# Kernel optimization log

Hardware: AMD Instinct MI355X
Metric: run time of the kernel (lower is better)

The kernel has to match this reference:

```python
import jax, jax.numpy as jnp
import numpy as np

B = 1024        # graphs per batch
NPG = 64        # nodes per graph (uniform)
DEG = 16        # avg degree
NE_PG = 256     # candidate non-edges per graph
N = B * NPG
E = N * DEG
NE = B * NE_PG
EMB, HID, NCAT, NET, NOUT = 64, 128, 100, 4, 101  # NOUT = num_external + 1


def setup_inputs() -> dict:
    key = jax.random.key(0)
    ks = jax.random.split(key, 32)
    rn = lambda k, shape: jax.random.normal(k, shape, jnp.float32) * 0.05
    # graph structure: edges and non-edges stay within each graph's node block
    x = jax.random.randint(ks[0], (N,), 0, NCAT)
    offs = jnp.repeat(jnp.arange(B) * NPG, NPG * DEG)
    src = jax.random.randint(ks[1], (E,), 0, NPG) + offs
    dst = jax.random.randint(ks[2], (E,), 0, NPG) + offs
    edge_index = jnp.stack([src, dst])
    edge_attr = jax.random.randint(ks[3], (E,), 0, NET)
    offs_ne = jnp.repeat(jnp.arange(B) * NPG, NE_PG)
    non_edges = jax.random.randint(ks[4], (NE, 2), 0, NPG) + offs_ne[:, None]
    batch = jnp.repeat(jnp.arange(B), NPG)
    return dict(
        node_tab=rn(ks[5], (NCAT, EMB)), edge_tab=rn(ks[6], (NET, EMB)),
        c1_w=rn(ks[7], (EMB, HID)), c1_we=rn(ks[8], (EMB, HID)),
        c1_as=rn(ks[9], (HID,)), c1_ad=rn(ks[10], (HID,)), c1_ae=rn(ks[11], (HID,)), c1_b=rn(ks[12], (HID,)),
        c2_w=rn(ks[13], (HID, HID)), c2_we=rn(ks[14], (EMB, HID)),
        c2_as=rn(ks[15], (HID,)), c2_ad=rn(ks[16], (HID,)), c2_ae=rn(ks[17], (HID,)), c2_b=rn(ks[18], (HID,)),
        s_w1=rn(ks[19], (HID, HID)), s_b1=rn(ks[20], (HID,)), s_w2=rn(ks[21], (HID, 1)), s_b2=rn(ks[22], (1,)),
        n_w1=rn(ks[23], (HID, HID)), n_b1=rn(ks[24], (HID,)), n_w2=rn(ks[25], (HID, NOUT)), n_b2=rn(ks[26], (NOUT,)),
        e_w1=rn(ks[27], (HID, HID)), e_b1=rn(ks[28], (HID,)), e_w2=rn(ks[29], (HID, 1)), e_b2=rn(ks[30], (1,)),
        x=x, edge_index=edge_index, edge_attr=edge_attr, non_edges=non_edges, batch=batch,
    )


def _gat(h_in, src, dst, e, W, We, a_s, a_d, a_e, b):
    """PyG GATConv, heads=1: gather -> leakyrelu logits -> segment softmax over dst -> scatter sum."""
    n = h_in.shape[0]
    h = h_in @ W                  # [N, C]
    he = e @ We                   # [E, C]
    logit = (h @ a_s)[src] + (h @ a_d)[dst] + he @ a_e   # [E]
    logit = jnp.where(logit > 0, logit, 0.2 * logit)      # leaky_relu(0.2)
    m = jax.ops.segment_max(logit, dst, num_segments=n)
    ex = jnp.exp(logit - m[dst])
    den = jax.ops.segment_sum(ex, dst, num_segments=n)
    alpha = ex / (den[dst] + 1e-16)
    return jax.ops.segment_sum(h[src] * alpha[:, None], dst, num_segments=n) + b


def _mlp(z, w1, b1, w2, b2):
    return jax.nn.relu(z @ w1 + b1) @ w2 + b2


def reference(node_tab, edge_tab,
              c1_w, c1_we, c1_as, c1_ad, c1_ae, c1_b,
              c2_w, c2_we, c2_as, c2_ad, c2_ae, c2_b,
              s_w1, s_b1, s_w2, s_b2,
              n_w1, n_b1, n_w2, n_b2,
              e_w1, e_b1, e_w2, e_b2,
              x, edge_index, edge_attr, non_edges, batch):
    src, dst = edge_index[0], edge_index[1]
    e = edge_tab[edge_attr]                      # [E, EMB]
    h = node_tab[x]                              # [N, EMB]
    h = jax.nn.relu(_gat(h, src, dst, e, c1_w, c1_we, c1_as, c1_ad, c1_ae, c1_b))
    h = _gat(h, src, dst, e, c2_w, c2_we, c2_as, c2_ad, c2_ae, c2_b)   # [N, HID]
    g = jax.ops.segment_sum(h, batch, num_segments=B)                   # [B, HID]
    stop = _mlp(g, s_w1, s_b1, s_w2, s_b2)                              # [B, 1]
    addnode = _mlp(h, n_w1, n_b1, n_w2, n_b2)                           # [N, NOUT]
    pair = h[non_edges[:, 0]] + h[non_edges[:, 1]]                      # [NE, HID]
    addedge = _mlp(pair, e_w1, e_b1, e_w2, e_b2)                        # [NE, 1]
    # uniform per-graph sizes -> the torch split/pad is a static reshape+concat
    return jnp.concatenate(
        [stop, addnode.reshape(B, NPG * NOUT), addedge.reshape(B, NE_PG)], axis=1)
```

## Files before the change

### kernel.cpp

```cpp
#include <hip/hip_runtime.h>


#define NPG 64
#define EPG 1024
#define NEPG 256
#define B_GR 1024
#define E_TOT 1048576
#define EMB 64
#define HID 128
#define NOUT 101
#define OUT_PG 6721

typedef __attribute__((ext_vector_type(8))) short bf16x8;
typedef __attribute__((ext_vector_type(4))) float f32x4;
typedef unsigned short ushort_t;

__device__ ushort_t g_c1w[EMB*HID];
__device__ ushort_t g_c2w[HID*HID];
__device__ ushort_t g_nw1[HID*HID];
__device__ ushort_t g_ew1[HID*HID];
__device__ ushort_t g_nw2[HID*112];
__device__ float    g_sw1t[HID*HID];
__device__ float    g_he1[4], g_he2[4];

__device__ __forceinline__ ushort_t f2bf(float f) {
  unsigned u = __float_as_uint(f);
  return (ushort_t)((u + 0x7fffu + ((u >> 16) & 1u)) >> 16);
}
__device__ __forceinline__ float bf2f(ushort_t h) {
  return __uint_as_float(((unsigned)h) << 16);
}

__global__ void prep_kernel(
    const float* __restrict__ edge_tab,
    const float* __restrict__ c1_w,  const float* __restrict__ c1_we,
    const float* __restrict__ c1_ae,
    const float* __restrict__ c2_w,  const float* __restrict__ c2_we,
    const float* __restrict__ c2_ae,
    const float* __restrict__ s_w1,  const float* __restrict__ n_w1,
    const float* __restrict__ n_w2,  const float* __restrict__ e_w1)
{
  const int b = blockIdx.x, tid = threadIdx.x;
  if (b == 0) {
    __shared__ float v1[EMB], v2[EMB];
    if (tid < EMB) {
      float a = 0.f, d = 0.f;
      for (int j = 0; j < HID; ++j) {
        a = fmaf(c1_we[tid*HID + j], c1_ae[j], a);
        d = fmaf(c2_we[tid*HID + j], c2_ae[j], d);
      }
      v1[tid] = a; v2[tid] = d;
    }
    __syncthreads();
    if (tid < 4) {
      float a = 0.f, d = 0.f;
      for (int k = 0; k < EMB; ++k) {
        const float ev = edge_tab[tid*EMB + k];
        a = fmaf(ev, v1[k], a); d = fmaf(ev, v2[k], d);
      }
      g_he1[tid] = a; g_he2[tid] = d;
    }
  } else if (b == 1) {
    for (int idx = tid; idx < EMB*HID; idx += 256) {
      const int j = idx & 7, l = (idx >> 3) & 63, r2 = idx >> 9;
      const int ks = r2 & 1, ct = r2 >> 1;
      const int row = ks*32 + (l >> 4)*8 + j;
      const int col = ct*16 + (l & 15);
      g_c1w[idx] = f2bf(c1_w[row*HID + col]);
    }
  } else if (b >= 2 && b <= 4) {
    const float* W = (b == 2) ? c2_w : (b == 3) ? n_w1 : e_w1;
    ushort_t* G = (b == 2) ? g_c2w : (b == 3) ? g_nw1 : g_ew1;
    for (int idx = tid; idx < HID*HID; idx += 256) {
      const int j = idx & 7, l = (idx >> 3) & 63, r2 = idx >> 9;
      const int ks = r2 & 3, ct = r2 >> 2;
      const int row = ks*32 + (l >> 4)*8 + j;
      const int col = ct*16 + (l & 15);
      G[idx] = f2bf(W[row*HID + col]);
    }
  } else if (b == 5) {
    for (int idx = tid; idx < HID*112; idx += 256) {
      const int j = idx & 7, l = (idx >> 3) & 63, r2 = idx >> 9;
      const int ks = r2 & 3, ct = r2 >> 2;
      const int row = ks*32 + (l >> 4)*8 + j;
      const int col = ct*16 + (l & 15);
      g_nw2[idx] = (col < NOUT) ? f2bf(n_w2[row*NOUT + col]) : (ushort_t)0;
    }
  } else {
    for (int idx = tid; idx < HID*HID; idx += 256)
      g_sw1t[idx] = s_w1[(idx & 127)*HID + (idx >> 7)];
  }
}

#define S_HC  0
#define S_R   18432
#define S_TP  35840
#define S_DEN 37888
#define S_NS  38144
#define S_ND  38400
#define S_XS  38656
#define S_GP  38912
#define S_ZH  39424
#define S_HCC 39936
#define S_TOT 39968

__global__ __launch_bounds__(256, 4) void graph_kernel(
    const float* __restrict__ node_tab,
    const float* __restrict__ c1_as, const float* __restrict__ c1_ad,
    const float* __restrict__ c1_b,
    const float* __restrict__ c2_as, const float* __restrict__ c2_ad,
    const float* __restrict__ c2_b,
    const float* __restrict__ s_b1,  const float* __restrict__ s_w2,
    const float* __restrict__ s_b2,
    const float* __restrict__ n_b1,  const float* __restrict__ n_b2,
    const float* __restrict__ e_b1,  const float* __restrict__ e_w2,
    const float* __restrict__ e_b2,
    const int* __restrict__ x,  const int* __restrict__ ei,
    const int* __restrict__ ea, const int* __restrict__ nedg,
    float* __restrict__ out)
{
  const int tid = threadIdx.x;
  const int gid = blockIdx.x;
  const int nb = gid * NPG;
  const int lane = tid & 63;
  const int wv = tid >> 6;
  const int qd = lane >> 4;
  const int cl = lane & 15;
  const int rb = wv * 16;

  __shared__ __align__(16) char smem[S_TOT];
  ushort_t* Hc   = (ushort_t*)(smem + S_HC);
  ushort_t* Ae   = (ushort_t*)(smem + S_R);
  float*    Pf   = (float*)   (smem + S_R);
  ushort_t* Pb   = (ushort_t*)(smem + S_R);
  ushort_t* Hr   = (ushort_t*)(smem + S_R);
  ushort_t* topo = (ushort_t*)(smem + S_TP);
  float*    part = (float*)   (smem + S_TP);
  float*    den  = (float*)   (smem + S_DEN);
  float*    ns   = (float*)   (smem + S_NS);
  float*    nd   = (float*)   (smem + S_ND);
  int*      xs   = (int*)     (smem + S_XS);
  float*    gp   = (float*)   (smem + S_GP);
  float*    zh   = (float*)   (smem + S_ZH);
  float*    hc   = (float*)   (smem + S_HCC);
  ushort_t* a1b  = Hc;

  for (int k = tid; k < EPG; k += 256) {
    const int s = ei[gid*EPG + k] - nb;
    const int d = ei[E_TOT + gid*EPG + k] - nb;
    const int t = ea[gid*EPG + k];
    topo[k] = (ushort_t)(s | (d << 6) | (t << 12));
  }
  if (tid < NPG) xs[tid] = x[nb + tid];
  if (tid >= 64 && tid < 72) hc[tid-64] = (tid < 68) ? g_he1[tid-64] : g_he2[tid-68];
  if (tid >= 128) gp[tid-128] = 0.f;
  __syncthreads();

  {
    const int n = tid >> 2;
    const int f0 = (tid & 3) * 16;
    const float* src = node_tab + xs[n]*EMB + f0;
    const float4 v0 = ((const float4*)src)[0];
    const float4 v1 = ((const float4*)src)[1];
    const float4 v2 = ((const float4*)src)[2];
    const float4 v3 = ((const float4*)src)[3];
    bf16x8 o0, o1;
    o0[0]=f2bf(v0.x); o0[1]=f2bf(v0.y); o0[2]=f2bf(v0.z); o0[3]=f2bf(v0.w);
    o0[4]=f2bf(v1.x); o0[5]=f2bf(v1.y); o0[6]=f2bf(v1.z); o0[7]=f2bf(v1.w);
    o1[0]=f2bf(v2.x); o1[1]=f2bf(v2.y); o1[2]=f2bf(v2.z); o1[3]=f2bf(v2.w);
    o1[4]=f2bf(v3.x); o1[5]=f2bf(v3.y); o1[6]=f2bf(v3.z); o1[7]=f2bf(v3.w);
    *(bf16x8*)(Ae + n*72 + f0)     = o0;
    *(bf16x8*)(Ae + n*72 + f0 + 8) = o1;
  }
  __syncthreads();

  {
    const bf16x8 af0 = *(const bf16x8*)(Ae + (rb+cl)*72 + qd*8);
    const bf16x8 af1 = *(const bf16x8*)(Ae + (rb+cl)*72 + 32 + qd*8);
    float pns[4] = {0.f,0.f,0.f,0.f}, pnd[4] = {0.f,0.f,0.f,0.f};
    #pragma unroll
    for (int ct = 0; ct < 8; ++ct) {
      f32x4 acc = {0.f, 0.f, 0.f, 0.f};
      const bf16x8 b0 = *(const bf16x8*)(g_c1w + ((ct*2+0)*64 + lane)*8);
      const bf16x8 b1 = *(const bf16x8*)(g_c1w + ((ct*2+1)*64 + lane)*8);
      acc = __builtin_amdgcn_mfma_f32_16x16x32_bf16(af0, b0, acc, 0, 0, 0);
      acc = __builtin_amdgcn_mfma_f32_16x16x32_bf16(af1, b1, acc, 0, 0, 0);
      const int n = ct*16 + cl;
      const float asv = c1_as[n], adv = c1_ad[n];
      #pragma unroll
      for (int r = 0; r < 4; ++r) {
        const float v = acc[r];
        Hc[n*72 + (rb + qd*4 + r)] = f2bf(v);
        pns[r] = fmaf(v, asv, pns[r]);
        pnd[r] = fmaf(v, adv, pnd[r]);
      }
    }
    #pragma unroll
    for (int r = 0; r < 4; ++r) {
      #pragma unroll
      for (int off = 1; off < 16; off <<= 1) {
        pns[r] += __shfl_xor(pns[r], off, 64);
        pnd[r] += __shfl_xor(pnd[r], off, 64);
      }
    }
    if (cl == 0) {
      #pragma unroll
      for (int r = 0; r < 4; ++r) { ns[rb+qd*4+r] = pns[r]; nd[rb+qd*4+r] = pnd[r]; }
    }
  }
  __syncthreads();

  {
    float4* pz = (float4*)Pf;
    #pragma unroll
    for (int j = 0; j < 4; ++j) pz[tid + j*256] = make_float4(0.f,0.f,0.f,0.f);
    if (tid < NPG) den[tid] = 0.f;
  }
  __syncthreads();

  for (int k = tid; k < EPG; k += 256) {
    const int tp = topo[k];
    const int s = tp & 63, d = (tp >> 6) & 63, t = tp >> 12;
    float l = ns[s] + nd[d] + hc[t];
    l = (l > 0.f) ? l : 0.2f * l;
    const float ex = __expf(l);
    atomicAdd(&den[d], ex);
    atomicAdd(&Pf[d*64 + s], ex);
  }
  __syncthreads();

  {
    float vreg[16];
    #pragma unroll
    for (int j = 0; j < 16; ++j) vreg[j] = Pf[tid + j*256];
    __syncthreads();
    #pragma unroll
    for (int j = 0; j < 16; ++j) {
      const int i = tid + j*256;
      Pb[(i >> 6)*72 + (i & 63)] = f2bf(vreg[j]);
    }
  }
  __syncthreads();

  {
    const bf16x8 a0 = *(const bf16x8*)(Pb + (rb+cl)*72 + qd*8);
    const bf16x8 a1 = *(const bf16x8*)(Pb + (rb+cl)*72 + 32 + qd*8);
    float inv4[4];
    #pragma unroll
    for (int r = 0; r < 4; ++r) inv4[r] = 1.f / (den[rb+qd*4+r] + 1e-16f);
    __syncthreads();
    #pragma unroll
    for (int ct = 0; ct < 8; ++ct) {
      f32x4 acc = {0.f, 0.f, 0.f, 0.f};
      const bf16x8 b0 = *(const bf16x8*)(Hc + (ct*16+cl)*72 + qd*8);
      const bf16x8 b1 = *(const bf16x8*)(Hc + (ct*16+cl)*72 + 32 + qd*8);
      acc = __builtin_amdgcn_mfma_f32_16x16x32_bf16(a0, b0, acc, 0, 0, 0);
      acc = __builtin_amdgcn_mfma_f32_16x16x32_bf16(a1, b1, acc, 0, 0, 0);
      const int n = ct*16 + cl;
      const float bias = c1_b[n];
      #pragma unroll
      for (int r = 0; r < 4; ++r)
        Hr[(rb + qd*4 + r)*136 + n] = f2bf(fmaxf(fmaf(acc[r], inv4[r], bias), 0.f));
    }
  }
  __syncthreads();

  {
    bf16x8 af[4];
    #pragma unroll
    for (int ks = 0; ks < 4; ++ks)
      af[ks] = *(const bf16x8*)(Hr + (rb+cl)*136 + ks*32 + qd*8);
    float pns[4] = {0.f,0.f,0.f,0.f}, pnd[4] = {0.f,0.f,0.f,0.f};
    #pragma unroll
    for (int ct = 0; ct < 8; ++ct) {
      f32x4 acc = {0.f, 0.f, 0.f, 0.f};
      #pragma unroll
      for (int ks = 0; ks < 4; ++ks) {
        const bf16x8 b = *(const bf16x8*)(g_c2w + ((ct*4+ks)*64 + lane)*8);
        acc = __builtin_amdgcn_mfma_f32_16x16x32_bf16(af[ks], b, acc, 0, 0, 0);
      }
      const int n = ct*16 + cl;
      const float asv = c2_as[n], adv = c2_ad[n];
      #pragma unroll
      for (int r = 0; r < 4; ++r) {
        const float v = acc[r];
        Hc[n*72 + (rb + qd*4 + r)] = f2bf(v);
        pns[r] = fmaf(v, asv, pns[r]);
        pnd[r] = fmaf(v, adv, pnd[r]);
      }
    }
    #pragma unroll
    for (int r = 0; r < 4; ++r) {
      #pragma unroll
      for (int off = 1; off < 16; off <<= 1) {
        pns[r] += __shfl_xor(pns[r], off, 64);
        pnd[r] += __shfl_xor(pnd[r], off, 64);
      }
    }
    if (cl == 0) {
      #pragma unroll
      for (int r = 0; r < 4; ++r) { ns[rb+qd*4+r] = pns[r]; nd[rb+qd*4+r] = pnd[r]; }
    }
  }
  __syncthreads();

  {
    float4* pz = (float4*)Pf;
    #pragma unroll
    for (int j = 0; j < 4; ++j) pz[tid + j*256] = make_float4(0.f,0.f,0.f,0.f);
    if (tid < NPG) den[tid] = 0.f;
  }
  __syncthreads();

  for (int k = tid; k < EPG; k += 256) {
    const int tp = topo[k];
    const int s = tp & 63, d = (tp >> 6) & 63, t = tp >> 12;
    float l = ns[s] + nd[d] + hc[4 + t];
    l = (l > 0.f) ? l : 0.2f * l;
    const float ex = __expf(l);
    atomicAdd(&den[d], ex);
    atomicAdd(&Pf[d*64 + s], ex);
  }
  __syncthreads();

  {
    float vreg[16];
    #pragma unroll
    for (int j = 0; j < 16; ++j) vreg[j] = Pf[tid + j*256];
    __syncthreads();
    #pragma unroll
    for (int j = 0; j < 16; ++j) {
      const int i = tid + j*256;
      Pb[(i >> 6)*72 + (i & 63)] = f2bf(vreg[j]);
    }
  }
  __syncthreads();

  {
    const bf16x8 a0 = *(const bf16x8*)(Pb + (rb+cl)*72 + qd*8);
    const bf16x8 a1 = *(const bf16x8*)(Pb + (rb+cl)*72 + 32 + qd*8);
    float inv4[4];
    #pragma unroll
    for (int r = 0; r < 4; ++r) inv4[r] = 1.f / (den[rb+qd*4+r] + 1e-16f);
    __syncthreads();
    #pragma unroll
    for (int ct = 0; ct < 8; ++ct) {
      f32x4 acc = {0.f, 0.f, 0.f, 0.f};
      const bf16x8 b0 = *(const bf16x8*)(Hc + (ct*16+cl)*72 + qd*8);
      const bf16x8 b1 = *(const bf16x8*)(Hc + (ct*16+cl)*72 + 32 + qd*8);
      acc = __builtin_amdgcn_mfma_f32_16x16x32_bf16(a0, b0, acc, 0, 0, 0);
      acc = __builtin_amdgcn_mfma_f32_16x16x32_bf16(a1, b1, acc, 0, 0, 0);
      const int n = ct*16 + cl;
      const float bias = c2_b[n];
      float colsum = 0.f;
      #pragma unroll
      for (int r = 0; r < 4; ++r) {
        const float v = fmaf(acc[r], inv4[r], bias);
        Hr[(rb + qd*4 + r)*136 + n] = f2bf(v);
        colsum += v;
      }
      colsum += __shfl_xor(colsum, 16, 64);
      colsum += __shfl_xor(colsum, 32, 64);
      if (qd == 0) atomicAdd(&gp[n], colsum);
    }
  }
  __syncthreads();

  {
    const int j = tid & 127, half = tid >> 7;
    const float* wr = g_sw1t + j*HID + half*64;
    const float* gr = gp + half*64;
    float p = 0.f;
    #pragma unroll
    for (int q = 0; q < 16; ++q) {
      const float4 w = ((const float4*)wr)[q];
      const float4 g = ((const float4*)gr)[q];
      p = fmaf(w.x, g.x, p); p = fmaf(w.y, g.y, p);
      p = fmaf(w.z, g.z, p); p = fmaf(w.w, g.w, p);
    }
    part[tid] = p;
  }
  __syncthreads();
  if (tid < HID) zh[tid] = fmaxf(part[tid] + part[tid+128] + s_b1[tid], 0.f);
  __syncthreads();
  if (tid < 64) {
    float p = fmaf(zh[tid], s_w2[tid], zh[tid+64]*s_w2[tid+64]);
    #pragma unroll
    for (int off = 32; off > 0; off >>= 1) p += __shfl_down(p, off, 64);
    if (tid == 0) out[(size_t)gid*OUT_PG] = p + s_b2[0];
  }
  __syncthreads();

  {
    bf16x8 af[4];
    #pragma unroll
    for (int ks = 0; ks < 4; ++ks)
      af[ks] = *(const bf16x8*)(Hr + (rb+cl)*136 + ks*32 + qd*8);
    #pragma unroll
    for (int ct = 0; ct < 8; ++ct) {
      f32x4 acc = {0.f, 0.f, 0.f, 0.f};
      #pragma unroll
      for (int ks = 0; ks < 4; ++ks) {
        const bf16x8 b = *(const bf16x8*)(g_nw1 + ((ct*4+ks)*64 + lane)*8);
        acc = __builtin_amdgcn_mfma_f32_16x16x32_bf16(af[ks], b, acc, 0, 0, 0);
      }
      const int n = ct*16 + cl;
      const float bias = n_b1[n];
      #pragma unroll
      for (int r = 0; r < 4; ++r)
        a1b[(rb + qd*4 + r)*136 + n] = f2bf(fmaxf(acc[r] + bias, 0.f));
    }
  }
  __syncthreads();

  {
    bf16x8 af[4];
    #pragma unroll
    for (int ks = 0; ks < 4; ++ks)
      af[ks] = *(const bf16x8*)(a1b + (rb+cl)*136 + ks*32 + qd*8);
    float* ob = out + (size_t)gid*OUT_PG + 1;
    #pragma unroll
    for (int ct = 0; ct < 7; ++ct) {
      f32x4 acc = {0.f, 0.f, 0.f, 0.f};
      #pragma unroll
      for (int ks = 0; ks < 4; ++ks) {
        const bf16x8 b = *(const bf16x8*)(g_nw2 + ((ct*4+ks)*64 + lane)*8);
        acc = __builtin_amdgcn_mfma_f32_16x16x32_bf16(af[ks], b, acc, 0, 0, 0);
      }
      const int o = ct*16 + cl;
      if (o < NOUT) {
        const float b2 = n_b2[o];
        #pragma unroll
        for (int r = 0; r < 4; ++r)
          ob[(size_t)(rb + qd*4 + r)*NOUT + o] = acc[r] + b2;
      }
    }
  }
  __syncthreads();

  if (tid < HID) { gp[tid] = e_b1[tid]; zh[tid] = e_w2[tid]; }
  {
    bf16x8 af[4];
    #pragma unroll
    for (int ks = 0; ks < 4; ++ks)
      af[ks] = *(const bf16x8*)(Hr + (rb+cl)*136 + ks*32 + qd*8);
    #pragma unroll
    for (int ct = 0; ct < 8; ++ct) {
      f32x4 acc = {0.f, 0.f, 0.f, 0.f};
      #pragma unroll
      for (int ks = 0; ks < 4; ++ks) {
        const bf16x8 b = *(const bf16x8*)(g_ew1 + ((ct*4+ks)*64 + lane)*8);
        acc = __builtin_amdgcn_mfma_f32_16x16x32_bf16(af[ks], b, acc, 0, 0, 0);
      }
      const int n = ct*16 + cl;
      #pragma unroll
      for (int r = 0; r < 4; ++r)
        a1b[(rb + qd*4 + r)*136 + n] = f2bf(acc[r]);
    }
  }
  __syncthreads();

  {
    const int2 pr = *(const int2*)(nedg + 2*(gid*NEPG + tid));
    const ushort_t* ui = a1b + (pr.x - nb)*136;
    const ushort_t* uj = a1b + (pr.y - nb)*136;
    float ssum = 0.f;
    #pragma unroll
    for (int q8 = 0; q8 < 16; ++q8) {
      const bf16x8 va = *(const bf16x8*)(ui + q8*8);
      const bf16x8 vb = *(const bf16x8*)(uj + q8*8);
      #pragma unroll
      for (int j = 0; j < 8; ++j) {
        const int c = q8*8 + j;
        float v = bf2f((ushort_t)va[j]) + bf2f((ushort_t)vb[j]) + gp[c];
        v = fmaxf(v, 0.f);
        ssum = fmaf(v, zh[c], ssum);
      }
    }
    out[(size_t)gid*OUT_PG + 1 + NPG*NOUT + tid] = ssum + e_b2[0];
  }
}

extern "C" void kernel_launch(void* const* d_in, const int* in_sizes, int n_in,
                              void* d_out, int out_size, void* d_ws, size_t ws_size,
                              hipStream_t stream) {
  const float* node_tab = (const float*)d_in[0];
  const float* edge_tab = (const float*)d_in[1];
  const float* c1_w  = (const float*)d_in[2];
  const float* c1_we = (const float*)d_in[3];
  const float* c1_as = (const float*)d_in[4];
  const float* c1_ad = (const float*)d_in[5];
  const float* c1_ae = (const float*)d_in[6];
  const float* c1_b  = (const float*)d_in[7];
  const float* c2_w  = (const float*)d_in[8];
  const float* c2_we = (const float*)d_in[9];
  const float* c2_as = (const float*)d_in[10];
  const float* c2_ad = (const float*)d_in[11];
  const float* c2_ae = (const float*)d_in[12];
  const float* c2_b  = (const float*)d_in[13];
  const float* s_w1  = (const float*)d_in[14];
  const float* s_b1  = (const float*)d_in[15];
  const float* s_w2  = (const float*)d_in[16];
  const float* s_b2  = (const float*)d_in[17];
  const float* n_w1  = (const float*)d_in[18];
  const float* n_b1  = (const float*)d_in[19];
  const float* n_w2  = (const float*)d_in[20];
  const float* n_b2  = (const float*)d_in[21];
  const float* e_w1  = (const float*)d_in[22];
  const float* e_b1  = (const float*)d_in[23];
  const float* e_w2  = (const float*)d_in[24];
  const float* e_b2  = (const float*)d_in[25];
  const int* x    = (const int*)d_in[26];
  const int* ei   = (const int*)d_in[27];
  const int* ea   = (const int*)d_in[28];
  const int* nedg = (const int*)d_in[29];
  float* out = (float*)d_out;

  prep_kernel<<<dim3(7), dim3(256), 0, stream>>>(
      edge_tab, c1_w, c1_we, c1_ae, c2_w, c2_we, c2_ae,
      s_w1, n_w1, n_w2, e_w1);

  graph_kernel<<<dim3(B_GR), dim3(256), 0, stream>>>(
      node_tab, c1_as, c1_ad, c1_b, c2_as, c2_ad, c2_b,
      s_b1, s_w2, s_b2, n_b1, n_b2, e_b1, e_w2, e_b2,
      x, ei, ea, nedg, out);
}
```

Measured before the change: 205.8 us.

## Keep edges and fragments in registers and drop redundant barriers and LDS passes

Each thread now keeps its packed edge topology in registers instead of an LDS array. Node embeddings are loaded straight into MFMA A-fragments, skipping a staging pass through shared memory. The fp32 attention matrix is read and converted to bf16 directly into fragments, and the softmax denominator comes from row sums via wave shuffles, which removes the den atomics and the separate bf16 repack pass. Several barriers are removed where each wave only touches its own rows, cutting sync overhead and LDS footprint; the cost is more register pressure and reliance on wave-local ordering for correctness.

```diff
diff --git a/kernel.cpp b/kernel.cpp
--- a/kernel.cpp
+++ b/kernel.cpp
@@ -92,17 +92,15 @@
   }
 }
 
-#define S_HC  0
-#define S_R   18432
-#define S_TP  35840
-#define S_DEN 37888
-#define S_NS  38144
-#define S_ND  38400
-#define S_XS  38656
-#define S_GP  38912
-#define S_ZH  39424
-#define S_HCC 39936
-#define S_TOT 39968
+#define S_HC   0
+#define S_R    18432
+#define S_PART 35840
+#define S_NS   36864
+#define S_ND   37120
+#define S_GP   37376
+#define S_ZH   37888
+#define S_HCC  38400
+#define S_TOT  38432
 
 __global__ __launch_bounds__(256, 4) void graph_kernel(
     const float* __restrict__ node_tab,
@@ -130,61 +128,55 @@
 
   __shared__ __align__(16) char smem[S_TOT];
   ushort_t* Hc   = (ushort_t*)(smem + S_HC);
-  ushort_t* Ae   = (ushort_t*)(smem + S_R);
   float*    Pf   = (float*)   (smem + S_R);
-  ushort_t* Pb   = (ushort_t*)(smem + S_R);
   ushort_t* Hr   = (ushort_t*)(smem + S_R);
-  ushort_t* topo = (ushort_t*)(smem + S_TP);
-  float*    part = (float*)   (smem + S_TP);
-  float*    den  = (float*)   (smem + S_DEN);
+  float*    part = (float*)   (smem + S_PART);
   float*    ns   = (float*)   (smem + S_NS);
   float*    nd   = (float*)   (smem + S_ND);
-  int*      xs   = (int*)     (smem + S_XS);
   float*    gp   = (float*)   (smem + S_GP);
   float*    zh   = (float*)   (smem + S_ZH);
   float*    hc   = (float*)   (smem + S_HCC);
   ushort_t* a1b  = Hc;
 
-  for (int k = tid; k < EPG; k += 256) {
+  unsigned er[4];
+  #pragma unroll
+  for (int i = 0; i < 4; ++i) {
+    const int k = tid + 256*i;
     const int s = ei[gid*EPG + k] - nb;
     const int d = ei[E_TOT + gid*EPG + k] - nb;
     const int t = ea[gid*EPG + k];
-    topo[k] = (ushort_t)(s | (d << 6) | (t << 12));
-  }
-  if (tid < NPG) xs[tid] = x[nb + tid];
-  if (tid >= 64 && tid < 72) hc[tid-64] = (tid < 68) ? g_he1[tid-64] : g_he2[tid-68];
-  if (tid >= 128) gp[tid-128] = 0.f;
-  __syncthreads();
-
-  {
-    const int n = tid >> 2;
-    const int f0 = (tid & 3) * 16;
-    const float* src = node_tab + xs[n]*EMB + f0;
-    const float4 v0 = ((const float4*)src)[0];
-    const float4 v1 = ((const float4*)src)[1];
-    const float4 v2 = ((const float4*)src)[2];
-    const float4 v3 = ((const float4*)src)[3];
-    bf16x8 o0, o1;
-    o0[0]=f2bf(v0.x); o0[1]=f2bf(v0.y); o0[2]=f2bf(v0.z); o0[3]=f2bf(v0.w);
-    o0[4]=f2bf(v1.x); o0[5]=f2bf(v1.y); o0[6]=f2bf(v1.z); o0[7]=f2bf(v1.w);
-    o1[0]=f2bf(v2.x); o1[1]=f2bf(v2.y); o1[2]=f2bf(v2.z); o1[3]=f2bf(v2.w);
-    o1[4]=f2bf(v3.x); o1[5]=f2bf(v3.y); o1[6]=f2bf(v3.z); o1[7]=f2bf(v3.w);
-    *(bf16x8*)(Ae + n*72 + f0)     = o0;
-    *(bf16x8*)(Ae + n*72 + f0 + 8) = o1;
-  }
-  __syncthreads();
-
-  {
-    const bf16x8 af0 = *(const bf16x8*)(Ae + (rb+cl)*72 + qd*8);
-    const bf16x8 af1 = *(const bf16x8*)(Ae + (rb+cl)*72 + 32 + qd*8);
+    er[i] = (unsigned)(s | (d << 6) | (t << 12));
+  }
+  bf16x8 ea0, ea1;
+  {
+    const int cat = x[nb + rb + cl];
+    const float* src = node_tab + cat*EMB;
+    const float4 v0 = *(const float4*)(src + qd*8);
+    const float4 v1 = *(const float4*)(src + qd*8 + 4);
+    const float4 v2 = *(const float4*)(src + 32 + qd*8);
+    const float4 v3 = *(const float4*)(src + 36 + qd*8);
+    ea0[0]=f2bf(v0.x); ea0[1]=f2bf(v0.y); ea0[2]=f2bf(v0.z); ea0[3]=f2bf(v0.w);
+    ea0[4]=f2bf(v1.x); ea0[5]=f2bf(v1.y); ea0[6]=f2bf(v1.z); ea0[7]=f2bf(v1.w);
+    ea1[0]=f2bf(v2.x); ea1[1]=f2bf(v2.y); ea1[2]=f2bf(v2.z); ea1[3]=f2bf(v2.w);
+    ea1[4]=f2bf(v3.x); ea1[5]=f2bf(v3.y); ea1[6]=f2bf(v3.z); ea1[7]=f2bf(v3.w);
+  }
+  {
+    float4* pz = (float4*)Pf;
+    #pragma unroll
+    for (int j = 0; j < 4; ++j) pz[tid + j*256] = make_float4(0.f,0.f,0.f,0.f);
+  }
+  if (tid < 128) gp[tid] = 0.f;
+  if (tid < 8) hc[tid] = (tid < 4) ? g_he1[tid] : g_he2[tid-4];
+
+  {
     float pns[4] = {0.f,0.f,0.f,0.f}, pnd[4] = {0.f,0.f,0.f,0.f};
     #pragma unroll
     for (int ct = 0; ct < 8; ++ct) {
       f32x4 acc = {0.f, 0.f, 0.f, 0.f};
       const bf16x8 b0 = *(const bf16x8*)(g_c1w + ((ct*2+0)*64 + lane)*8);
       const bf16x8 b1 = *(const bf16x8*)(g_c1w + ((ct*2+1)*64 + lane)*8);
-      acc = __builtin_amdgcn_mfma_f32_16x16x32_bf16(af0, b0, acc, 0, 0, 0);
-      acc = __builtin_amdgcn_mfma_f32_16x16x32_bf16(af1, b1, acc, 0, 0, 0);
+      acc = __builtin_amdgcn_mfma_f32_16x16x32_bf16(ea0, b0, acc, 0, 0, 0);
+      acc = __builtin_amdgcn_mfma_f32_16x16x32_bf16(ea1, b1, acc, 0, 0, 0);
       const int n = ct*16 + cl;
       const float asv = c1_as[n], adv = c1_ad[n];
       #pragma unroll
@@ -210,52 +202,46 @@
   }
   __syncthreads();
 
-  {
-    float4* pz = (float4*)Pf;
-    #pragma unroll
-    for (int j = 0; j < 4; ++j) pz[tid + j*256] = make_float4(0.f,0.f,0.f,0.f);
-    if (tid < NPG) den[tid] = 0.f;
-  }
-  __syncthreads();
-
-  for (int k = tid; k < EPG; k += 256) {
-    const int tp = topo[k];
+  #pragma unroll
+  for (int i = 0; i < 4; ++i) {
+    const unsigned tp = er[i];
     const int s = tp & 63, d = (tp >> 6) & 63, t = tp >> 12;
     float l = ns[s] + nd[d] + hc[t];
     l = (l > 0.f) ? l : 0.2f * l;
-    const float ex = __expf(l);
-    atomicAdd(&den[d], ex);
-    atomicAdd(&Pf[d*64 + s], ex);
-  }
-  __syncthreads();
-
-  {
-    float vreg[16];
-    #pragma unroll
-    for (int j = 0; j < 16; ++j) vreg[j] = Pf[tid + j*256];
-    __syncthreads();
-    #pragma unroll
-    for (int j = 0; j < 16; ++j) {
-      const int i = tid + j*256;
-      Pb[(i >> 6)*72 + (i & 63)] = f2bf(vreg[j]);
-    }
-  }
-  __syncthreads();
-
-  {
-    const bf16x8 a0 = *(const bf16x8*)(Pb + (rb+cl)*72 + qd*8);
-    const bf16x8 a1 = *(const bf16x8*)(Pb + (rb+cl)*72 + 32 + qd*8);
-    float inv4[4];
-    #pragma unroll
-    for (int r = 0; r < 4; ++r) inv4[r] = 1.f / (den[rb+qd*4+r] + 1e-16f);
-    __syncthreads();
+    atomicAdd(&Pf[d*64 + s], __expf(l));
+  }
+  __syncthreads();
+
+  bf16x8 pa0, pa1;
+  float inv4[4];
+  {
+    const float* pr = Pf + (rb + cl)*64;
+    const float4 v0 = *(const float4*)(pr + qd*8);
+    const float4 v1 = *(const float4*)(pr + qd*8 + 4);
+    const float4 v2 = *(const float4*)(pr + 32 + qd*8);
+    const float4 v3 = *(const float4*)(pr + 36 + qd*8);
+    pa0[0]=f2bf(v0.x); pa0[1]=f2bf(v0.y); pa0[2]=f2bf(v0.z); pa0[3]=f2bf(v0.w);
+    pa0[4]=f2bf(v1.x); pa0[5]=f2bf(v1.y); pa0[6]=f2bf(v1.z); pa0[7]=f2bf(v1.w);
+    pa1[0]=f2bf(v2.x); pa1[1]=f2bf(v2.y); pa1[2]=f2bf(v2.z); pa1[3]=f2bf(v2.w);
+    pa1[4]=f2bf(v3.x); pa1[5]=f2bf(v3.y); pa1[6]=f2bf(v3.z); pa1[7]=f2bf(v3.w);
+    float den = v0.x+v0.y+v0.z+v0.w + v1.x+v1.y+v1.z+v1.w
+              + v2.x+v2.y+v2.z+v2.w + v3.x+v3.y+v3.z+v3.w;
+    den += __shfl_xor(den, 16, 64);
+    den += __shfl_xor(den, 32, 64);
+    #pragma unroll
+    for (int r = 0; r < 4; ++r)
+      inv4[r] = 1.f / (__shfl(den, qd*4 + r, 64) + 1e-16f);
+  }
+  __syncthreads();
+
+  {
     #pragma unroll
     for (int ct = 0; ct < 8; ++ct) {
       f32x4 acc = {0.f, 0.f, 0.f, 0.f};
       const bf16x8 b0 = *(const bf16x8*)(Hc + (ct*16+cl)*72 + qd*8);
       const bf16x8 b1 = *(const bf16x8*)(Hc + (ct*16+cl)*72 + 32 + qd*8);
-      acc = __builtin_amdgcn_mfma_f32_16x16x32_bf16(a0, b0, acc, 0, 0, 0);
-      acc = __builtin_amdgcn_mfma_f32_16x16x32_bf16(a1, b1, acc, 0, 0, 0);
+      acc = __builtin_amdgcn_mfma_f32_16x16x32_bf16(pa0, b0, acc, 0, 0, 0);
+      acc = __builtin_amdgcn_mfma_f32_16x16x32_bf16(pa1, b1, acc, 0, 0, 0);
       const int n = ct*16 + cl;
       const float bias = c1_b[n];
       #pragma unroll
@@ -263,13 +249,16 @@
         Hr[(rb + qd*4 + r)*136 + n] = f2bf(fmaxf(fmaf(acc[r], inv4[r], bias), 0.f));
     }
   }
-  __syncthreads();
-
-  {
-    bf16x8 af[4];
-    #pragma unroll
-    for (int ks = 0; ks < 4; ++ks)
-      af[ks] = *(const bf16x8*)(Hr + (rb+cl)*136 + ks*32 + qd*8);
+  bf16x8 h1f[4];
+  #pragma unroll
+  for (int ks = 0; ks < 4; ++ks)
+    h1f[ks] = *(const bf16x8*)(Hr + (rb+cl)*136 + ks*32 + qd*8);
+  __syncthreads();
+
+  {
+    float4* pz = (float4*)Pf;
+    #pragma unroll
+    for (int j = 0; j < 4; ++j) pz[tid + j*256] = make_float4(0.f,0.f,0.f,0.f);
     float pns[4] = {0.f,0.f,0.f,0.f}, pnd[4] = {0.f,0.f,0.f,0.f};
     #pragma unroll
     for (int ct = 0; ct < 8; ++ct) {
@@ -277,7 +266,7 @@
       #pragma unroll
       for (int ks = 0; ks < 4; ++ks) {
         const bf16x8 b = *(const bf16x8*)(g_c2w + ((ct*4+ks)*64 + lane)*8);
-        acc = __builtin_amdgcn_mfma_f32_16x16x32_bf16(af[ks], b, acc, 0, 0, 0);
+        acc = __builtin_amdgcn_mfma_f32_16x16x32_bf16(h1f[ks], b, acc, 0, 0, 0);
       }
       const int n = ct*16 + cl;
       const float asv = c2_as[n], adv = c2_ad[n];
@@ -304,52 +293,44 @@
   }
   __syncthreads();
 
-  {
-    float4* pz = (float4*)Pf;
-    #pragma unroll
-    for (int j = 0; j < 4; ++j) pz[tid + j*256] = make_float4(0.f,0.f,0.f,0.f);
-    if (tid < NPG) den[tid] = 0.f;
-  }
-  __syncthreads();
-
-  for (int k = tid; k < EPG; k += 256) {
-    const int tp = topo[k];
+  #pragma unroll
+  for (int i = 0; i < 4; ++i) {
+    const unsigned tp = er[i];
     const int s = tp & 63, d = (tp >> 6) & 63, t = tp >> 12;
     float l = ns[s] + nd[d] + hc[4 + t];
     l = (l > 0.f) ? l : 0.2f * l;
-    const float ex = __expf(l);
-    atomicAdd(&den[d], ex);
-    atomicAdd(&Pf[d*64 + s], ex);
-  }
-  __syncthreads();
-
-  {
-    float vreg[16];
-    #pragma unroll
-    for (int j = 0; j < 16; ++j) vreg[j] = Pf[tid + j*256];
-    __syncthreads();
-    #pragma unroll
-    for (int j = 0; j < 16; ++j) {
-      const int i = tid + j*256;
-      Pb[(i >> 6)*72 + (i & 63)] = f2bf(vreg[j]);
-    }
-  }
-  __syncthreads();
-
-  {
-    const bf16x8 a0 = *(const bf16x8*)(Pb + (rb+cl)*72 + qd*8);
-    const bf16x8 a1 = *(const bf16x8*)(Pb + (rb+cl)*72 + 32 + qd*8);
-    float inv4[4];
-    #pragma unroll
-    for (int r = 0; r < 4; ++r) inv4[r] = 1.f / (den[rb+qd*4+r] + 1e-16f);
-    __syncthreads();
+    atomicAdd(&Pf[d*64 + s], __expf(l));
+  }
+  __syncthreads();
+
+  {
+    const float* pr = Pf + (rb + cl)*64;
+    const float4 v0 = *(const float4*)(pr + qd*8);
+    const float4 v1 = *(const float4*)(pr + qd*8 + 4);
+    const float4 v2 = *(const float4*)(pr + 32 + qd*8);
+    const float4 v3 = *(const float4*)(pr + 36 + qd*8);
+    pa0[0]=f2bf(v0.x); pa0[1]=f2bf(v0.y); pa0[2]=f2bf(v0.z); pa0[3]=f2bf(v0.w);
+    pa0[4]=f2bf(v1.x); pa0[5]=f2bf(v1.y); pa0[6]=f2bf(v1.z); pa0[7]=f2bf(v1.w);
+    pa1[0]=f2bf(v2.x); pa1[1]=f2bf(v2.y); pa1[2]=f2bf(v2.z); pa1[3]=f2bf(v2.w);
+    pa1[4]=f2bf(v3.x); pa1[5]=f2bf(v3.y); pa1[6]=f2bf(v3.z); pa1[7]=f2bf(v3.w);
+    float den = v0.x+v0.y+v0.z+v0.w + v1.x+v1.y+v1.z+v1.w
+              + v2.x+v2.y+v2.z+v2.w + v3.x+v3.y+v3.z+v3.w;
+    den += __shfl_xor(den, 16, 64);
+    den += __shfl_xor(den, 32, 64);
+    #pragma unroll
+    for (int r = 0; r < 4; ++r)
+      inv4[r] = 1.f / (__shfl(den, qd*4 + r, 64) + 1e-16f);
+  }
+  __syncthreads();
+
+  {
     #pragma unroll
     for (int ct = 0; ct < 8; ++ct) {
       f32x4 acc = {0.f, 0.f, 0.f, 0.f};
       const bf16x8 b0 = *(const bf16x8*)(Hc + (ct*16+cl)*72 + qd*8);
       const bf16x8 b1 = *(const bf16x8*)(Hc + (ct*16+cl)*72 + 32 + qd*8);
-      acc = __builtin_amdgcn_mfma_f32_16x16x32_bf16(a0, b0, acc, 0, 0, 0);
-      acc = __builtin_amdgcn_mfma_f32_16x16x32_bf16(a1, b1, acc, 0, 0, 0);
+      acc = __builtin_amdgcn_mfma_f32_16x16x32_bf16(pa0, b0, acc, 0, 0, 0);
+      acc = __builtin_amdgcn_mfma_f32_16x16x32_bf16(pa1, b1, acc, 0, 0, 0);
       const int n = ct*16 + cl;
       const float bias = c2_b[n];
       float colsum = 0.f;
@@ -383,26 +364,28 @@
   __syncthreads();
   if (tid < HID) zh[tid] = fmaxf(part[tid] + part[tid+128] + s_b1[tid], 0.f);
   __syncthreads();
+
   if (tid < 64) {
     float p = fmaf(zh[tid], s_w2[tid], zh[tid+64]*s_w2[tid+64]);
     #pragma unroll
     for (int off = 32; off > 0; off >>= 1) p += __shfl_down(p, off, 64);
     if (tid == 0) out[(size_t)gid*OUT_PG] = p + s_b2[0];
   }
-  __syncthreads();
-
-  {
-    bf16x8 af[4];
-    #pragma unroll
-    for (int ks = 0; ks < 4; ++ks)
-      af[ks] = *(const bf16x8*)(Hr + (rb+cl)*136 + ks*32 + qd*8);
+  part[tid] = (tid < 128) ? e_b1[tid] : e_w2[tid-128];
+
+  bf16x8 h2f[4];
+  #pragma unroll
+  for (int ks = 0; ks < 4; ++ks)
+    h2f[ks] = *(const bf16x8*)(Hr + (rb+cl)*136 + ks*32 + qd*8);
+
+  {
     #pragma unroll
     for (int ct = 0; ct < 8; ++ct) {
       f32x4 acc = {0.f, 0.f, 0.f, 0.f};
       #pragma unroll
       for (int ks = 0; ks < 4; ++ks) {
         const bf16x8 b = *(const bf16x8*)(g_nw1 + ((ct*4+ks)*64 + lane)*8);
-        acc = __builtin_amdgcn_mfma_f32_16x16x32_bf16(af[ks], b, acc, 0, 0, 0);
+        acc = __builtin_amdgcn_mfma_f32_16x16x32_bf16(h2f[ks], b, acc, 0, 0, 0);
       }
       const int n = ct*16 + cl;
       const float bias = n_b1[n];
@@ -411,8 +394,6 @@
         a1b[(rb + qd*4 + r)*136 + n] = f2bf(fmaxf(acc[r] + bias, 0.f));
     }
   }
-  __syncthreads();
-
   {
     bf16x8 af[4];
     #pragma unroll
@@ -436,21 +417,14 @@
       }
     }
   }
-  __syncthreads();
-
-  if (tid < HID) { gp[tid] = e_b1[tid]; zh[tid] = e_w2[tid]; }
-  {
-    bf16x8 af[4];
-    #pragma unroll
-    for (int ks = 0; ks < 4; ++ks)
-      af[ks] = *(const bf16x8*)(Hr + (rb+cl)*136 + ks*32 + qd*8);
+  {
     #pragma unroll
     for (int ct = 0; ct < 8; ++ct) {
       f32x4 acc = {0.f, 0.f, 0.f, 0.f};
       #pragma unroll
       for (int ks = 0; ks < 4; ++ks) {
         const bf16x8 b = *(const bf16x8*)(g_ew1 + ((ct*4+ks)*64 + lane)*8);
-        acc = __builtin_amdgcn_mfma_f32_16x16x32_bf16(af[ks], b, acc, 0, 0, 0);
+        acc = __builtin_amdgcn_mfma_f32_16x16x32_bf16(h2f[ks], b, acc, 0, 0, 0);
       }
       const int n = ct*16 + cl;
       #pragma unroll
@@ -472,9 +446,9 @@
       #pragma unroll
       for (int j = 0; j < 8; ++j) {
         const int c = q8*8 + j;
-        float v = bf2f((ushort_t)va[j]) + bf2f((ushort_t)vb[j]) + gp[c];
+        float v = bf2f((ushort_t)va[j]) + bf2f((ushort_t)vb[j]) + part[c];
         v = fmaxf(v, 0.f);
-        ssum = fmaf(v, zh[c], ssum);
+        ssum = fmaf(v, part[128 + c], ssum);
       }
     }
     out[(size_t)gid*OUT_PG + 1 + NPG*NOUT + tid] = ssum + e_b2[0];
```

New measurement: 201.6 us. 2.0% less time.
